# Performance work log

Measured on AMD Instinct MI355X. Metric: run time of the kernel, lower is better.

The kernel has to match this reference:

```python
import jax, jax.numpy as jnp
import numpy as np

B, T, C = 1, 2048, 4096
H, HS, NE = 32, 128, 32  # n_head, head_size, rope_n_elem


def setup_inputs() -> dict:
    key = jax.random.key(0)
    ks = jax.random.split(key, 7)
    sd = 1.0 / np.sqrt(C)
    return {
        "x": jax.random.normal(ks[0], (B, T, C), jnp.float32),
        "cos": jax.random.uniform(ks[1], (T, NE), jnp.float32, -1.0, 1.0),
        "sin": jax.random.uniform(ks[2], (T, NE), jnp.float32, -1.0, 1.0),
        "W_attn": jax.random.normal(ks[3], (3 * C, C), jnp.float32) * sd,
        "b_attn": jax.random.normal(ks[4], (3 * C,), jnp.float32) * 0.01,
        "W_proj": jax.random.normal(ks[5], (C, C), jnp.float32) * sd,
        "b_proj": jax.random.normal(ks[6], (C,), jnp.float32) * 0.01,
    }


def _apply_rope(t, cos, sin):
    # t: (B,H,T,HS); rope only on first NE dims
    tr, tp = t[..., :NE], t[..., NE:]
    x1, x2 = tr[..., : NE // 2], tr[..., NE // 2 :]
    rotated = jnp.concatenate([-x2, x1], axis=-1)
    c = cos[None, :, :]  # (1,T,NE) broadcasts over (B,H,T,NE)
    s = sin[None, :, :]
    return jnp.concatenate([tr * c + rotated * s, tp], axis=-1)


def reference(x, cos, sin, W_attn, b_attn, W_proj, b_proj):
    b, t, c = x.shape
    qkv = x @ W_attn.T + b_attn  # (B,T,3C)
    # view (B,T,G,total_qkv,HS) then permute -> (B,G,total_qkv,T,HS); G=H, q_per_kv=1
    qkv = qkv.reshape(b, t, H, 3, HS).transpose(0, 2, 3, 1, 4)
    q, k, v = qkv[:, :, 0], qkv[:, :, 1], qkv[:, :, 2]  # each (B,H,T,HS)
    q = _apply_rope(q, cos, sin)
    k = _apply_rope(k, cos, sin)
    scale = 1.0 / jnp.sqrt(jnp.asarray(HS, x.dtype))
    scores = jnp.einsum("bhqd,bhkd->bhqk", q, k) * scale
    causal = jnp.tril(jnp.ones((t, t), bool))
    scores = jnp.where(causal, scores, -jnp.inf)
    attn = jax.nn.softmax(scores, axis=-1)
    y = jnp.einsum("bhqk,bhkd->bhqd", attn, v)
    y = y.transpose(0, 2, 1, 3).reshape(b, t, H * HS)
    return y @ W_proj.T + b_proj
```

## Files before the change

### kernel.cpp

```cpp
#include <hip/hip_runtime.h>
#include <cstdint>
#include <cstddef>

typedef __bf16 bf16x8 __attribute__((ext_vector_type(8)));
typedef __bf16 bf16x4 __attribute__((ext_vector_type(4)));
typedef float fx4 __attribute__((ext_vector_type(4)));

static constexpr int T = 2048;
static constexpr int C = 4096;
static constexpr int H = 32;
static constexpr int HS = 128;
static constexpr int QKV_N = 12288;

#define MFMA16(a, b, c) __builtin_amdgcn_mfma_f32_16x16x32_bf16((a), (b), (c), 0, 0, 0)

__device__ __forceinline__ void async_cp16(const void* g, void* l) {
  __builtin_amdgcn_global_load_lds((const __attribute__((address_space(1))) unsigned int*)g,
                                   (__attribute__((address_space(3))) unsigned int*)l,
                                   16, 0, 0);
}

__global__ __launch_bounds__(256) void cvt_f32_to_bf16(const float* __restrict__ in,
                                                       __bf16* __restrict__ out, int n4) {
  int i = blockIdx.x * 256 + threadIdx.x;
  if (i >= n4) return;
  float4 v = ((const float4*)in)[i];
  bf16x4 o;
  o.x = (__bf16)v.x; o.y = (__bf16)v.y; o.z = (__bf16)v.z; o.w = (__bf16)v.w;
  ((bf16x4*)out)[i] = o;
}

template <int OUT_BF16>
__global__ __launch_bounds__(256, 2) void gemm_bt(const __bf16* __restrict__ A,
                                                  const __bf16* __restrict__ B,
                                                  const float* __restrict__ bias,
                                                  void* __restrict__ Cout,
                                                  int M, int N, int K) {
  constexpr int BM = 128, BN = 128, BK = 64;
  __shared__ __align__(16) __bf16 As[BM * BK];
  __shared__ __align__(16) __bf16 Bs[BN * BK];
  const int tid = threadIdx.x;
  const int lane = tid & 63;
  const int wid = tid >> 6;
  const int wm = (wid >> 1) * 64;
  const int wn = (wid & 1) * 64;
  const int m0 = blockIdx.y * BM;
  const int n0 = blockIdx.x * BN;
  const int lr = lane & 15;
  const int quad = lane >> 4;

  fx4 acc[4][4] = {};

  for (int k0 = 0; k0 < K; k0 += BK) {
#pragma unroll
    for (int c = 0; c < 4; ++c) {
      int chunk = wid * 4 + c;
      int s = chunk * 64 + lane;
      int r = s >> 3;
      int kc = (s & 7) ^ (r & 7);
      async_cp16(A + (size_t)(m0 + r) * K + k0 + kc * 8, &As[chunk * 512]);
      async_cp16(B + (size_t)(n0 + r) * K + k0 + kc * 8, &Bs[chunk * 512]);
    }
    __syncthreads();
#pragma unroll
    for (int ks = 0; ks < BK; ks += 32) {
      bf16x8 af[4], bfr[4];
#pragma unroll
      for (int mm = 0; mm < 4; ++mm) {
        int r = wm + mm * 16 + lr;
        int kc = (ks >> 3) + quad;
        af[mm] = *(const bf16x8*)(&As[(r * 8 + (kc ^ (r & 7))) * 8]);
      }
#pragma unroll
      for (int nn = 0; nn < 4; ++nn) {
        int r = wn + nn * 16 + lr;
        int kc = (ks >> 3) + quad;
        bfr[nn] = *(const bf16x8*)(&Bs[(r * 8 + (kc ^ (r & 7))) * 8]);
      }
#pragma unroll
      for (int mm = 0; mm < 4; ++mm)
#pragma unroll
        for (int nn = 0; nn < 4; ++nn)
          acc[mm][nn] = MFMA16(af[mm], bfr[nn], acc[mm][nn]);
    }
    __syncthreads();
  }

#pragma unroll
  for (int nn = 0; nn < 4; ++nn) {
    int col = n0 + wn + nn * 16 + lr;
    float bv = bias[col];
#pragma unroll
    for (int mm = 0; mm < 4; ++mm) {
#pragma unroll
      for (int r = 0; r < 4; ++r) {
        int row = m0 + wm + mm * 16 + quad * 4 + r;
        float v = acc[mm][nn][r] + bv;
        if (OUT_BF16)
          ((__bf16*)Cout)[(size_t)row * N + col] = (__bf16)v;
        else
          ((float*)Cout)[(size_t)row * N + col] = v;
      }
    }
  }
}

__global__ __launch_bounds__(256) void rope_kernel(__bf16* __restrict__ qkv,
                                                   const float* __restrict__ cosp,
                                                   const float* __restrict__ sinp) {
  int tid = blockIdx.x * 256 + threadIdx.x;
  int d = tid & 15;
  int which = (tid >> 4) & 1;
  int h = (tid >> 5) & 31;
  int t = tid >> 10;
  size_t base = (size_t)t * QKV_N + h * 384 + which * 128;
  float x1 = (float)qkv[base + d];
  float x2 = (float)qkv[base + d + 16];
  float c1 = cosp[t * 32 + d], s1 = sinp[t * 32 + d];
  float c2 = cosp[t * 32 + d + 16], s2 = sinp[t * 32 + d + 16];
  qkv[base + d] = (__bf16)(x1 * c1 - x2 * s1);
  qkv[base + d + 16] = (__bf16)(x2 * c2 + x1 * s2);
}

__global__ __launch_bounds__(256) void vtrans_kernel(const __bf16* __restrict__ qkv,
                                                     __bf16* __restrict__ vt) {
  __shared__ __align__(16) __bf16 tile[64][136];
  int h = blockIdx.x;
  int t0 = blockIdx.y * 64;
  int tid = threadIdx.x;
#pragma unroll
  for (int c = 0; c < 4; ++c) {
    int i = tid + c * 256;
    int tl = i >> 4;
    int dp = (i & 15) * 8;
    *(uint4*)(&tile[tl][dp]) = *(const uint4*)(qkv + (size_t)(t0 + tl) * QKV_N + h * 384 + 256 + dp);
  }
  __syncthreads();
#pragma unroll
  for (int c = 0; c < 4; ++c) {
    int o = tid + c * 256;
    int d = o >> 3;
    int ts = (o & 7) * 8;
    bf16x8 v;
#pragma unroll
    for (int j = 0; j < 8; ++j) v[j] = tile[ts + j][d];
    *(bf16x8*)(vt + ((size_t)h * 128 + d) * T + t0 + ts) = v;
  }
}

__global__ __launch_bounds__(256, 2) void attn_kernel(const __bf16* __restrict__ qkv,
                                                      const __bf16* __restrict__ vt,
                                                      __bf16* __restrict__ y) {
  constexpr int KT = 64;
  constexpr int LPS = KT + 8;
  __shared__ __align__(16) __bf16 Ks[KT * HS];
  __shared__ __align__(16) __bf16 Vs[HS * KT];
  __shared__ __align__(16) __bf16 Ps[4][16 * LPS];

  const int h = blockIdx.x;
  const int qb = blockIdx.y;
  const int q0 = qb * 64;
  const int tid = threadIdx.x;
  const int lane = tid & 63;
  const int wid = tid >> 6;
  const int lr = lane & 15;
  const int quad = lane >> 4;
  const int qrow = q0 + wid * 16;

  bf16x8 qf[4];
#pragma unroll
  for (int kk = 0; kk < 4; ++kk)
    qf[kk] = *(const bf16x8*)(qkv + (size_t)(qrow + lr) * QKV_N + h * 384 + kk * 32 + quad * 8);

  float lsum[4];
  fx4 acc_o[8];
#pragma unroll
  for (int r = 0; r < 4; ++r) lsum[r] = 0.f;
#pragma unroll
  for (int dd = 0; dd < 8; ++dd) acc_o[dd] = (fx4)0.f;

  const float c_e2 = 0.08838834764831845f * 1.4426950408889634f;
  const int ntiles = qb + 1;
  for (int kt = 0; kt < ntiles; ++kt) {
    const int kbase = kt * KT;
#pragma unroll
    for (int c = 0; c < 4; ++c) {
      int chunk = wid * 4 + c;
      int s = chunk * 64 + lane;
      int r = s >> 4;
      int kc = (s & 15) ^ (r & 15);
      async_cp16(qkv + (size_t)(kbase + r) * QKV_N + h * 384 + 128 + kc * 8, &Ks[chunk * 512]);
    }
#pragma unroll
    for (int c = 0; c < 4; ++c) {
      int chunk = wid * 4 + c;
      int s = chunk * 64 + lane;
      int r = s >> 3;
      int kc = (s & 7) ^ (r & 7);
      async_cp16(vt + ((size_t)h * 128 + r) * T + kbase + kc * 8, &Vs[chunk * 512]);
    }
    __syncthreads();

    fx4 sv[4] = {};
#pragma unroll
    for (int nn = 0; nn < 4; ++nn) {
#pragma unroll
      for (int kk = 0; kk < 4; ++kk) {
        int r = nn * 16 + lr;
        int kc = kk * 4 + quad;
        bf16x8 kf = *(const bf16x8*)(&Ks[(r * 16 + (kc ^ (r & 15))) * 8]);
        sv[nn] = MFMA16(qf[kk], kf, sv[nn]);
      }
    }

#pragma unroll
    for (int nn = 0; nn < 4; ++nn) {
      int kj = kbase + nn * 16 + lr;
#pragma unroll
      for (int r = 0; r < 4; ++r) {
        int qi = qrow + quad * 4 + r;
        float p = __builtin_amdgcn_exp2f(sv[nn][r] * c_e2);
        p = (kj > qi) ? 0.f : p;
        lsum[r] += p;
        Ps[wid][(quad * 4 + r) * LPS + nn * 16 + lr] = (__bf16)p;
      }
    }
    asm volatile("s_waitcnt lgkmcnt(0)" ::: "memory");

#pragma unroll
    for (int kc0 = 0; kc0 < 2; ++kc0) {
      bf16x8 pf = *(const bf16x8*)(&Ps[wid][lr * LPS + kc0 * 32 + quad * 8]);
#pragma unroll
      for (int dd = 0; dd < 8; ++dd) {
        int r = dd * 16 + lr;
        int kc = kc0 * 4 + quad;
        bf16x8 vf = *(const bf16x8*)(&Vs[(r * 8 + (kc ^ (r & 7))) * 8]);
        acc_o[dd] = MFMA16(pf, vf, acc_o[dd]);
      }
    }
    __syncthreads();
  }

#pragma unroll
  for (int off = 1; off < 16; off <<= 1)
#pragma unroll
    for (int r = 0; r < 4; ++r)
      lsum[r] += __shfl_xor(lsum[r], off, 64);
#pragma unroll
  for (int r = 0; r < 4; ++r) lsum[r] = 1.0f / lsum[r];

#pragma unroll
  for (int dd = 0; dd < 8; ++dd)
#pragma unroll
    for (int r = 0; r < 4; ++r) {
      int row = qrow + quad * 4 + r;
      int col = h * 128 + dd * 16 + lr;
      y[(size_t)row * C + col] = (__bf16)(acc_o[dd][r] * lsum[r]);
    }
}

extern "C" void kernel_launch(void* const* d_in, const int* in_sizes, int n_in,
                              void* d_out, int out_size, void* d_ws, size_t ws_size,
                              hipStream_t stream) {
  const float* x      = (const float*)d_in[0];
  const float* cosp   = (const float*)d_in[1];
  const float* sinp   = (const float*)d_in[2];
  const float* W_attn = (const float*)d_in[3];
  const float* b_attn = (const float*)d_in[4];
  const float* W_proj = (const float*)d_in[5];
  const float* b_proj = (const float*)d_in[6];
  float* out = (float*)d_out;

  char* wsb = (char*)d_ws;
  __bf16* Wab  = (__bf16*)(wsb + 0);
  __bf16* Wpb  = (__bf16*)(wsb + 100663296);
  __bf16* xb   = (__bf16*)(wsb + 134217728);
  __bf16* qkvb = (__bf16*)(wsb + 150994944);
  __bf16* yb   = (__bf16*)(wsb + 201326592);
  __bf16* vtb  = (__bf16*)(wsb + 218103808);

  cvt_f32_to_bf16<<<8192, 256, 0, stream>>>(x, xb, (T * C) / 4);
  cvt_f32_to_bf16<<<49152, 256, 0, stream>>>(W_attn, Wab, (QKV_N * C) / 4);
  cvt_f32_to_bf16<<<16384, 256, 0, stream>>>(W_proj, Wpb, (C * C) / 4);

  gemm_bt<1><<<dim3(96, 16), 256, 0, stream>>>(xb, Wab, b_attn, (void*)qkvb, T, QKV_N, C);

  rope_kernel<<<8192, 256, 0, stream>>>(qkvb, cosp, sinp);
  vtrans_kernel<<<dim3(32, 32), 256, 0, stream>>>(qkvb, vtb);

  attn_kernel<<<dim3(32, 32), 256, 0, stream>>>(qkvb, vtb, yb);

  gemm_bt<0><<<dim3(32, 16), 256, 0, stream>>>(yb, Wpb, b_proj, (void*)out, T, C, C);
}
```

Measured before the change: 740.1 us.

## Add 256x256 pipelined GEMM kernel for QKV projection

Introduces a new 512-thread GEMM kernel with 256x256 output tiles, double-buffered half-K LDS staging through async global-to-LDS loads, explicit barriers and waitcnts that overlap loads with MFMA phases, XOR-swizzled LDS layout, and a workgroup swizzle. It replaces the 128-tile GEMM for the QKV projection to raise data reuse and hide memory latency. The cost is higher register and LDS pressure per workgroup (128KB LDS), and a grid of only 384 workgroups, which may underfill the GPU.

```diff
diff --git a/kernel.cpp b/kernel.cpp
--- a/kernel.cpp
+++ b/kernel.cpp
@@ -105,6 +105,140 @@
   }
 }
 
+__device__ __forceinline__ void stage_half_256(const __bf16* __restrict__ src,
+                                               __bf16* lds, int row0, int kcol0,
+                                               int K, int tid) {
+#pragma unroll
+  for (int j2 = 0; j2 < 2; ++j2) {
+    int s = j2 * 512 + tid;
+    int r = s >> 2;
+    int kc = (s & 3) ^ (r & 3);
+    async_cp16(src + (size_t)(row0 + r) * K + kcol0 + kc * 8,
+               lds + (size_t)(j2 * 512 + (tid & 448)) * 8);
+  }
+}
+
+#define GBAR()                                  \
+  do {                                          \
+    __builtin_amdgcn_sched_barrier(0);          \
+    asm volatile("s_barrier" ::: "memory");     \
+    __builtin_amdgcn_sched_barrier(0);          \
+  } while (0)
+
+#define PHASE(P, KK, MMB, LOADB, STAGE_STMT, TAILWAIT)                          \
+  {                                                                             \
+    const __bf16* Ah = &As[P][KK][0];                                           \
+    const __bf16* Bh = &Bs[P][KK][0];                                           \
+    bf16x8 af[4];                                                               \
+    _Pragma("unroll") for (int m_ = 0; m_ < 4; ++m_) {                          \
+      int r_ = (wr << 7) + (MMB + m_) * 16 + lr;                                \
+      af[m_] = *(const bf16x8*)(Ah + ((r_ << 2) + (quad ^ (r_ & 3))) * 8);      \
+    }                                                                           \
+    if (LOADB) {                                                                \
+      _Pragma("unroll") for (int n_ = 0; n_ < 4; ++n_) {                        \
+        int r_ = (wc << 6) + n_ * 16 + lr;                                      \
+        bfr[n_] = *(const bf16x8*)(Bh + ((r_ << 2) + (quad ^ (r_ & 3))) * 8);   \
+      }                                                                         \
+    }                                                                           \
+    STAGE_STMT;                                                                 \
+    GBAR();                                                                     \
+    asm volatile("s_waitcnt lgkmcnt(0)" ::: "memory");                          \
+    __builtin_amdgcn_sched_barrier(0);                                          \
+    __builtin_amdgcn_s_setprio(1);                                              \
+    _Pragma("unroll") for (int m_ = 0; m_ < 4; ++m_)                            \
+      _Pragma("unroll") for (int n_ = 0; n_ < 4; ++n_)                          \
+        acc[MMB + m_][n_] = MFMA16(af[m_], bfr[n_], acc[MMB + m_][n_]);         \
+    __builtin_amdgcn_s_setprio(0);                                              \
+    TAILWAIT;                                                                   \
+    GBAR();                                                                     \
+  }
+
+template <int OUT_BF16>
+__global__ __launch_bounds__(512, 2) void gemm_bt_256(const __bf16* __restrict__ A,
+                                                      const __bf16* __restrict__ B,
+                                                      const float* __restrict__ bias,
+                                                      void* __restrict__ Cout,
+                                                      int M, int N, int K) {
+  __shared__ __align__(16) __bf16 As[2][2][8192];
+  __shared__ __align__(16) __bf16 Bs[2][2][8192];
+  const int tid = threadIdx.x;
+  const int lane = tid & 63;
+  const int wid = tid >> 6;
+  const int wr = wid >> 2;
+  const int wc = wid & 3;
+  const int lr = lane & 15;
+  const int quad = lane >> 4;
+
+  int nwg = gridDim.x * gridDim.y;
+  int orig = blockIdx.y * gridDim.x + blockIdx.x;
+  int swz = orig;
+  if ((nwg & 7) == 0) swz = (orig & 7) * (nwg >> 3) + (orig >> 3);
+  const int m0 = (swz / gridDim.x) * 256;
+  const int n0 = (swz % gridDim.x) * 256;
+
+  fx4 acc[8][4] = {};
+  bf16x8 bfr[4];
+
+  const int NT = K >> 6;
+  const int NPAIR = NT >> 1;
+
+  stage_half_256(B, &Bs[0][0][0], n0, 0, K, tid);
+  stage_half_256(A, &As[0][0][0], m0, 0, K, tid);
+  stage_half_256(B, &Bs[0][1][0], n0, 32, K, tid);
+  stage_half_256(A, &As[0][1][0], m0, 32, K, tid);
+  asm volatile("s_waitcnt vmcnt(4)" ::: "memory");
+  stage_half_256(B, &Bs[1][0][0], n0, 64, K, tid);
+  stage_half_256(A, &As[1][0][0], m0, 64, K, tid);
+  stage_half_256(B, &Bs[1][1][0], n0, 96, K, tid);
+  asm volatile("s_waitcnt vmcnt(6)" ::: "memory");
+  GBAR();
+
+  for (int i = 0; i + 1 < NPAIR; ++i) {
+    const int k1 = (2 * i + 1) << 6;
+    const int k2 = (2 * i + 2) << 6;
+    const int k3 = (2 * i + 3) << 6;
+    PHASE(0, 0, 0, 1, stage_half_256(A, &As[1][1][0], m0, k1 + 32, K, tid), );
+    PHASE(0, 0, 4, 0, stage_half_256(B, &Bs[0][0][0], n0, k2, K, tid), );
+    PHASE(0, 1, 0, 1, stage_half_256(A, &As[0][0][0], m0, k2, K, tid), );
+    PHASE(0, 1, 4, 0, stage_half_256(B, &Bs[0][1][0], n0, k2 + 32, K, tid),
+          asm volatile("s_waitcnt vmcnt(6)" ::: "memory"));
+    PHASE(1, 0, 0, 1, stage_half_256(A, &As[0][1][0], m0, k2 + 32, K, tid), );
+    PHASE(1, 0, 4, 0, stage_half_256(B, &Bs[1][0][0], n0, k3, K, tid), );
+    PHASE(1, 1, 0, 1, stage_half_256(A, &As[1][0][0], m0, k3, K, tid), );
+    PHASE(1, 1, 4, 0, stage_half_256(B, &Bs[1][1][0], n0, k3 + 32, K, tid),
+          asm volatile("s_waitcnt vmcnt(6)" ::: "memory"));
+  }
+  {
+    const int k1 = (NT - 1) << 6;
+    PHASE(0, 0, 0, 1, stage_half_256(A, &As[1][1][0], m0, k1 + 32, K, tid), );
+    PHASE(0, 0, 4, 0, , asm volatile("s_waitcnt vmcnt(4)" ::: "memory"));
+    PHASE(0, 1, 0, 1, , asm volatile("s_waitcnt vmcnt(2)" ::: "memory"));
+    PHASE(0, 1, 4, 0, , asm volatile("s_waitcnt vmcnt(0)" ::: "memory"));
+    PHASE(1, 0, 0, 1, , );
+    PHASE(1, 0, 4, 0, , );
+    PHASE(1, 1, 0, 1, , );
+    PHASE(1, 1, 4, 0, , );
+  }
+
+#pragma unroll
+  for (int nn = 0; nn < 4; ++nn) {
+    int col = n0 + (wc << 6) + nn * 16 + lr;
+    float bv = bias[col];
+#pragma unroll
+    for (int mm = 0; mm < 8; ++mm) {
+#pragma unroll
+      for (int r = 0; r < 4; ++r) {
+        int row = m0 + (wr << 7) + mm * 16 + quad * 4 + r;
+        float v = acc[mm][nn][r] + bv;
+        if (OUT_BF16)
+          ((__bf16*)Cout)[(size_t)row * N + col] = (__bf16)v;
+        else
+          ((float*)Cout)[(size_t)row * N + col] = v;
+      }
+    }
+  }
+}
+
 __global__ __launch_bounds__(256) void rope_kernel(__bf16* __restrict__ qkv,
                                                    const float* __restrict__ cosp,
                                                    const float* __restrict__ sinp) {
@@ -283,7 +417,7 @@
   cvt_f32_to_bf16<<<49152, 256, 0, stream>>>(W_attn, Wab, (QKV_N * C) / 4);
   cvt_f32_to_bf16<<<16384, 256, 0, stream>>>(W_proj, Wpb, (C * C) / 4);
 
-  gemm_bt<1><<<dim3(96, 16), 256, 0, stream>>>(xb, Wab, b_attn, (void*)qkvb, T, QKV_N, C);
+  gemm_bt_256<1><<<dim3(48, 8), 512, 0, stream>>>(xb, Wab, b_attn, (void*)qkvb, T, QKV_N, C);
 
   rope_kernel<<<8192, 256, 0, stream>>>(qkvb, cosp, sinp);
   vtrans_kernel<<<dim3(32, 32), 256, 0, stream>>>(qkvb, vtb);
```

Result: slower. 837.8 us (+13.2%).

## Double-buffer K/V tiles in attention kernel to overlap loads with compute

Applied to the files above, without the earlier changes.

Splits the attention loop into stage and compute phases and double-buffers the K and V shared-memory tiles. The next tile's async global-to-LDS copies are issued before computing the current tile, with vmcnt(8) waits so the in-flight prefetch is not waited on. This aims to hide global load latency behind the MFMA work. LDS use grows by 32KB per block, which may reduce occupancy under the 2-blocks-per-CU launch bound.

```diff
diff --git a/kernel.cpp b/kernel.cpp
--- a/kernel.cpp
+++ b/kernel.cpp
@@ -153,8 +153,8 @@
                                                       __bf16* __restrict__ y) {
   constexpr int KT = 64;
   constexpr int LPS = KT + 8;
-  __shared__ __align__(16) __bf16 Ks[KT * HS];
-  __shared__ __align__(16) __bf16 Vs[HS * KT];
+  __shared__ __align__(16) __bf16 Ks[2][KT * HS];
+  __shared__ __align__(16) __bf16 Vs[2][HS * KT];
   __shared__ __align__(16) __bf16 Ps[4][16 * LPS];
 
   const int h = blockIdx.x;
@@ -181,7 +181,8 @@
 
   const float c_e2 = 0.08838834764831845f * 1.4426950408889634f;
   const int ntiles = qb + 1;
-  for (int kt = 0; kt < ntiles; ++kt) {
+
+  auto stage = [&](int kt, int buf) {
     const int kbase = kt * KT;
 #pragma unroll
     for (int c = 0; c < 4; ++c) {
@@ -189,7 +190,8 @@
       int s = chunk * 64 + lane;
       int r = s >> 4;
       int kc = (s & 15) ^ (r & 15);
-      async_cp16(qkv + (size_t)(kbase + r) * QKV_N + h * 384 + 128 + kc * 8, &Ks[chunk * 512]);
+      async_cp16(qkv + (size_t)(kbase + r) * QKV_N + h * 384 + 128 + kc * 8,
+                 &Ks[buf][chunk * 512]);
     }
 #pragma unroll
     for (int c = 0; c < 4; ++c) {
@@ -197,10 +199,13 @@
       int s = chunk * 64 + lane;
       int r = s >> 3;
       int kc = (s & 7) ^ (r & 7);
-      async_cp16(vt + ((size_t)h * 128 + r) * T + kbase + kc * 8, &Vs[chunk * 512]);
-    }
-    __syncthreads();
-
+      async_cp16(vt + ((size_t)h * 128 + r) * T + kbase + kc * 8,
+                 &Vs[buf][chunk * 512]);
+    }
+  };
+
+  auto compute = [&](int kt, int buf) {
+    const int kbase = kt * KT;
     fx4 sv[4] = {};
 #pragma unroll
     for (int nn = 0; nn < 4; ++nn) {
@@ -208,7 +213,7 @@
       for (int kk = 0; kk < 4; ++kk) {
         int r = nn * 16 + lr;
         int kc = kk * 4 + quad;
-        bf16x8 kf = *(const bf16x8*)(&Ks[(r * 16 + (kc ^ (r & 15))) * 8]);
+        bf16x8 kf = *(const bf16x8*)(&Ks[buf][(r * 16 + (kc ^ (r & 15))) * 8]);
         sv[nn] = MFMA16(qf[kk], kf, sv[nn]);
       }
     }
@@ -234,12 +239,31 @@
       for (int dd = 0; dd < 8; ++dd) {
         int r = dd * 16 + lr;
         int kc = kc0 * 4 + quad;
-        bf16x8 vf = *(const bf16x8*)(&Vs[(r * 8 + (kc ^ (r & 7))) * 8]);
+        bf16x8 vf = *(const bf16x8*)(&Vs[buf][(r * 8 + (kc ^ (r & 7))) * 8]);
         acc_o[dd] = MFMA16(pf, vf, acc_o[dd]);
       }
     }
-    __syncthreads();
-  }
+  };
+
+  stage(0, 0);
+  int cur = 0;
+  for (int kt = 0; kt < ntiles - 1; ++kt) {
+    stage(kt + 1, cur ^ 1);
+    asm volatile("s_waitcnt vmcnt(8)" ::: "memory");
+    __builtin_amdgcn_sched_barrier(0);
+    __builtin_amdgcn_s_barrier();
+    __builtin_amdgcn_sched_barrier(0);
+    compute(kt, cur);
+    __builtin_amdgcn_sched_barrier(0);
+    __builtin_amdgcn_s_barrier();
+    __builtin_amdgcn_sched_barrier(0);
+    cur ^= 1;
+  }
+  asm volatile("s_waitcnt vmcnt(0)" ::: "memory");
+  __builtin_amdgcn_sched_barrier(0);
+  __builtin_amdgcn_s_barrier();
+  __builtin_amdgcn_sched_barrier(0);
+  compute(ntiles - 1, cur);
 
 #pragma unroll
   for (int off = 1; off < 16; off <<= 1)
```

Measured after the change: 733.4 us. About the same (-0.9%).
